# Kernel tuning notes

Hardware: AMD Instinct MI355X
Metric: run time of the kernel (lower is better)

## Reference

```python
import jax, jax.numpy as jnp
import numpy as np

EPS = 1e-8
LOSS_EPS = 1e-6
LOSS_WEIGHT = 1.0
N_BOXES = 262144

# ---------- rotated-2D-box helpers (mmcv diff_iou_rotated style) ----------

def box2corners_2d(box):
    # box: (N,5) = (x, y, w, h, alpha) -> corners (N,4,2), CCW order
    x, y, w, h, a = box[:, 0], box[:, 1], box[:, 2], box[:, 3], box[:, 4]
    x4 = jnp.array([0.5, -0.5, -0.5, 0.5], box.dtype) * w[:, None]   # (N,4)
    y4 = jnp.array([0.5, 0.5, -0.5, -0.5], box.dtype) * h[:, None]
    c, s = jnp.cos(a)[:, None], jnp.sin(a)[:, None]
    rx = x4 * c - y4 * s + x[:, None]
    ry = x4 * s + y4 * c + y[:, None]
    return jnp.stack([rx, ry], axis=-1)


def box_intersection(c1, c2):
    # segment-segment intersections between the 4 edges of each box
    # c1, c2: (N,4,2) -> pts (N,16,2), mask (N,16)
    l1 = jnp.concatenate([c1, jnp.roll(c1, -1, axis=1)], axis=-1)[:, :, None, :]  # (N,4,1,4)
    l2 = jnp.concatenate([c2, jnp.roll(c2, -1, axis=1)], axis=-1)[:, None, :, :]  # (N,1,4,4)
    x1, y1, x2, y2 = l1[..., 0], l1[..., 1], l1[..., 2], l1[..., 3]
    x3, y3, x4, y4 = l2[..., 0], l2[..., 1], l2[..., 2], l2[..., 3]
    num = (y4 - y3) * (x2 - x1) - (x4 - x3) * (y2 - y1)
    den_t = (x4 - x3) * (y1 - y3) - (y4 - y3) * (x1 - x3)
    den_u = (x2 - x1) * (y1 - y3) - (y2 - y1) * (x1 - x3)
    safe = jnp.where(num == 0.0, 1.0, num)
    t = jnp.where(num == 0.0, -1.0, den_t / safe)
    u = jnp.where(num == 0.0, -1.0, -den_u / safe)
    mask = (t > 0.0) & (t < 1.0) & (u > 0.0) & (u < 1.0)  # (N,4,4)
    t2 = den_t / (num + EPS)
    pts = jnp.stack([x1 + t2 * (x2 - x1), y1 + t2 * (y2 - y1)], axis=-1)
    pts = pts * mask[..., None]
    n = c1.shape[0]
    return pts.reshape(n, 16, 2), mask.reshape(n, 16)


def box_in_box(c1, c2):
    # which corners of box1 lie inside box2; c1,c2: (N,4,2) -> (N,4) bool
    a, b, d = c2[:, 0:1], c2[:, 1:2], c2[:, 3:4]
    ab, ad, am = b - a, d - a, c1 - a
    p_ab = jnp.sum(ab * am, -1) / jnp.sum(ab * ab, -1)
    p_ad = jnp.sum(ad * am, -1) / jnp.sum(ad * ad, -1)
    tol = 1e-6
    return (p_ab > -tol) & (p_ab < 1 + tol) & (p_ad > -tol) & (p_ad < 1 + tol)


def polygon_area(vertices, mask):
    # sort valid vertices CCW around their mean, close polygon, shoelace area
    # vertices: (N,24,2), mask: (N,24) bool -> area (N,)
    maskf = mask.astype(vertices.dtype)
    nv = jnp.maximum(jnp.sum(maskf, axis=1, keepdims=True), 1.0)
    mean = jnp.sum(vertices * maskf[..., None], axis=1, keepdims=True) / nv[..., None]
    v = vertices - mean
    ang = jnp.arctan2(v[..., 1], v[..., 0])
    # invalid vertices get huge, index-increasing keys so they sort last (stable)
    ang = jnp.where(mask, ang, 1e6 + jnp.arange(24, dtype=vertices.dtype))
    order = jnp.argsort(ang, axis=1)                         # (N,24) int
    vs = jnp.take_along_axis(v, order[..., None], axis=1)    # (N,24,2)
    ms = jnp.take_along_axis(mask, order, axis=1)
    first = vs[:, 0:1]                                       # first (valid) vertex
    vs = jnp.where(ms[..., None], vs, first)                 # pad closes polygon
    x, y = vs[..., 0], vs[..., 1]
    xn, yn = jnp.roll(x, -1, axis=1), jnp.roll(y, -1, axis=1)
    return 0.5 * jnp.abs(jnp.sum(x * yn - y * xn, axis=1))


def diff_iou_rotated_3d(b1, b2):
    # b1, b2: (N,7) = (x,y,z,w,h,l,alpha) -> IoU3D (N,)
    c1 = box2corners_2d(b1[:, jnp.array([0, 1, 3, 4, 6])])
    c2 = box2corners_2d(b2[:, jnp.array([0, 1, 3, 4, 6])])
    ipts, imask = box_intersection(c1, c2)
    m12 = box_in_box(c1, c2)
    m21 = box_in_box(c2, c1)
    vertices = jnp.concatenate([c1, c2, ipts], axis=1)   # (N,24,2)
    mask = jnp.concatenate([m12, m21, imask], axis=1)    # (N,24)
    inter_2d = polygon_area(vertices, mask)
    zmax1, zmin1 = b1[:, 2] + 0.5 * b1[:, 5], b1[:, 2] - 0.5 * b1[:, 5]
    zmax2, zmin2 = b2[:, 2] + 0.5 * b2[:, 5], b2[:, 2] - 0.5 * b2[:, 5]
    z_ov = jnp.maximum(jnp.minimum(zmax1, zmax2) - jnp.maximum(zmin1, zmin2), 0.0)
    inter_3d = inter_2d * z_ov
    vol1 = b1[:, 3] * b1[:, 4] * b1[:, 5]
    vol2 = b2[:, 3] * b2[:, 4] * b2[:, 5]
    return inter_3d / (vol1 + vol2 - inter_3d)


def corners_from_bboxes3d(b):
    # (N,7) -> (N,8,3); rotation about axis=1 (mmdet3d rotation_3d_in_axis)
    corners_norm = jnp.array([[-0.5, -0.5, -0.5], [-0.5, -0.5, 0.5],
                              [-0.5, 0.5, 0.5], [-0.5, 0.5, -0.5],
                              [0.5, -0.5, -0.5], [0.5, -0.5, 0.5],
                              [0.5, 0.5, 0.5], [0.5, 0.5, -0.5]], b.dtype)
    corners = corners_norm[None] * b[:, None, 3:6]          # (N,8,3)
    c, s = jnp.cos(b[:, 6])[:, None], jnp.sin(b[:, 6])[:, None]
    x, y, z = corners[..., 0], corners[..., 1], corners[..., 2]
    xr = x * c + z * s
    zr = -x * s + z * c
    return jnp.stack([xr, y, zr], axis=-1) + b[:, None, :3]


def diou_3d_loss(pred, target):
    iou3d = jnp.nan_to_num(diff_iou_rotated_3d(pred, target), nan=0.0)
    ctd = jnp.sum((pred[:, :3] - target[:, :3]) ** 2, axis=-1)
    cnd = jnp.mean(jnp.sum((corners_from_bboxes3d(pred)
                            - corners_from_bboxes3d(target)) ** 2, axis=-1), axis=1)
    did = jnp.sum(target[:, 3:6] ** 2, axis=-1)
    return 1.0 - iou3d + (ctd + cnd) / (ctd + cnd + did + LOSS_EPS)


def setup_inputs() -> dict:
    key = jax.random.key(0)
    k1, k2, k3, k4, k5 = jax.random.split(key, 5)
    xy = jax.random.uniform(k1, (N_BOXES, 2), minval=-40.0, maxval=40.0)
    z = jax.random.uniform(k2, (N_BOXES, 1), minval=-3.0, maxval=1.0)
    dims = jax.random.uniform(k3, (N_BOXES, 3), minval=0.8, maxval=4.0)
    ang = jax.random.uniform(k4, (N_BOXES, 1), minval=-np.pi, maxval=np.pi)
    target = jnp.concatenate([xy, z, dims, ang], axis=1).astype(jnp.float32)
    noise = jax.random.normal(k5, (N_BOXES, 7), jnp.float32) * \
        jnp.array([0.3, 0.3, 0.1, 0.2, 0.2, 0.2, 0.1], jnp.float32)
    pred = target + noise
    pred = pred.at[:, 3:6].set(jnp.maximum(pred[:, 3:6], 0.1))
    return {"pred": pred, "target": target}


def reference(pred, target):
    # DIOU3DLoss.forward with weight=None, reduction='mean'
    return LOSS_WEIGHT * jnp.mean(diou_3d_loss(pred, target))
```

## Files before the change

### kernel.cpp

```cpp
#include <hip/hip_runtime.h>
#include <math.h>

#define EPSI 1e-8f
#define TOLI 1e-6f

__device__ __forceinline__ float frcp(float x) { return __builtin_amdgcn_rcpf(x); }

#define CE(A, B) {                                  \
    unsigned ka = key[A], kb = key[B];              \
    key[A] = ka < kb ? ka : kb;                     \
    key[B] = ka < kb ? kb : ka; }

__global__ __launch_bounds__(256) void diou3d_main(
    const float* __restrict__ pred, const float* __restrict__ tgt,
    float* __restrict__ partial, int n)
{
    __shared__ float2 vbuf[24][256];
    __shared__ float wsum[4];
    int tx = threadIdx.x;
    int tid = blockIdx.x * 256 + tx;
    float loss = 0.0f;
    if (tid < n) {
        const float* P = pred + (size_t)tid * 7;
        const float* T = tgt  + (size_t)tid * 7;
        float p0 = P[0], p1 = P[1], p2 = P[2], p3 = P[3], p4 = P[4], p5 = P[5], p6 = P[6];
        float t0 = T[0], t1 = T[1], t2 = T[2], t3 = T[3], t4 = T[4], t5 = T[5], t6 = T[6];

        float sp, cp, st, ct;
        __sincosf(p6, &sp, &cp);
        __sincosf(t6, &st, &ct);
        const float hx[4] = {0.5f, -0.5f, -0.5f, 0.5f};
        const float hy[4] = {0.5f, 0.5f, -0.5f, -0.5f};
        float c1x[4], c1y[4], c2x[4], c2y[4];
#pragma unroll
        for (int k = 0; k < 4; k++) {
            float xa = hx[k] * p3, ya = hy[k] * p4;
            c1x[k] = xa * cp - ya * sp + p0;
            c1y[k] = xa * sp + ya * cp + p1;
            float xb = hx[k] * t3, yb = hy[k] * t4;
            c2x[k] = xb * ct - yb * st + t0;
            c2y[k] = xb * st + yb * ct + t1;
        }

        float vx[24], vy[24];
        bool  vm[24];

        {
            float abx = c2x[1] - c2x[0], aby = c2y[1] - c2y[0];
            float adx = c2x[3] - c2x[0], ady = c2y[3] - c2y[0];
            float rab = frcp(abx * abx + aby * aby);
            float rad = frcp(adx * adx + ady * ady);
#pragma unroll
            for (int k = 0; k < 4; k++) {
                float amx = c1x[k] - c2x[0], amy = c1y[k] - c2y[0];
                float pab = (abx * amx + aby * amy) * rab;
                float pad = (adx * amx + ady * amy) * rad;
                vm[k] = (pab > -TOLI) && (pab < 1.0f + TOLI) && (pad > -TOLI) && (pad < 1.0f + TOLI);
                vx[k] = c1x[k]; vy[k] = c1y[k];
            }
        }
        {
            float abx = c1x[1] - c1x[0], aby = c1y[1] - c1y[0];
            float adx = c1x[3] - c1x[0], ady = c1y[3] - c1y[0];
            float rab = frcp(abx * abx + aby * aby);
            float rad = frcp(adx * adx + ady * ady);
#pragma unroll
            for (int k = 0; k < 4; k++) {
                float amx = c2x[k] - c1x[0], amy = c2y[k] - c1y[0];
                float pab = (abx * amx + aby * amy) * rab;
                float pad = (adx * amx + ady * amy) * rad;
                vm[4 + k] = (pab > -TOLI) && (pab < 1.0f + TOLI) && (pad > -TOLI) && (pad < 1.0f + TOLI);
                vx[4 + k] = c2x[k]; vy[4 + k] = c2y[k];
            }
        }

#pragma unroll
        for (int i = 0; i < 4; i++) {
            float x1 = c1x[i], y1 = c1y[i];
            float dx12 = c1x[(i + 1) & 3] - x1, dy12 = c1y[(i + 1) & 3] - y1;
#pragma unroll
            for (int j = 0; j < 4; j++) {
                float x3 = c2x[j], y3 = c2y[j];
                float dx34 = c2x[(j + 1) & 3] - x3, dy34 = c2y[(j + 1) & 3] - y3;
                float num  = dy34 * dx12 - dx34 * dy12;
                float dxs = x1 - x3, dys = y1 - y3;
                float den_t = dx34 * dys - dy34 * dxs;
                float den_u = dx12 * dys - dy12 * dxs;
                bool m = (den_t * num > 0.0f) && ((num - den_t) * num > 0.0f)
                      && (den_u * num < 0.0f) && ((num + den_u) * num > 0.0f);
                float t2d = den_t * frcp(num + EPSI);
                int idx = 8 + i * 4 + j;
                vx[idx] = x1 + t2d * dx12;
                vy[idx] = y1 + t2d * dy12;
                vm[idx] = m;
            }
        }

        float cntf = 0.0f, sx = 0.0f, sy = 0.0f;
#pragma unroll
        for (int k = 0; k < 24; k++) {
            cntf += vm[k] ? 1.0f : 0.0f;
            sx   += vm[k] ? vx[k] : 0.0f;
            sy   += vm[k] ? vy[k] : 0.0f;
        }
        int ic = (int)cntf;
        float rnv = frcp(fmaxf(cntf, 1.0f));
        float mx = sx * rnv, my = sy * rnv;

        unsigned key[24];
#pragma unroll
        for (int k = 0; k < 24; k++) {
            float ux = vx[k] - mx, uy = vy[k] - my;
            vbuf[k][tx] = make_float2(ux, uy);
            float d = fabsf(ux) + fabsf(uy);
            float pq = ux * frcp(d);
            pq = (d == 0.0f) ? 0.0f : pq;
            float ang = (uy < 0.0f) ? (pq - 1.0f) : (1.0f - pq);
            unsigned u = __float_as_uint(ang);
            u ^= (unsigned)(((int)u >> 31)) | 0x80000000u;
            unsigned kk = (u & 0xFFFFFFE0u) | (unsigned)k;
            key[k] = vm[k] ? kk : (0xFFFFFFE0u | (unsigned)k);
        }

#pragma unroll
        for (int p = 1; p < 32; p <<= 1) {
#pragma unroll
            for (int k = p; k >= 1; k >>= 1) {
#pragma unroll
                for (int j = k & (p - 1); j + k < 32; j += 2 * k) {
#pragma unroll
                    for (int i = 0; i < k; i++) {
                        int lo = i + j, hi = i + j + k;
                        if (hi < 24 && (lo / (2 * p) == hi / (2 * p))) {
                            CE(lo, hi);
                        }
                    }
                }
            }
        }

        float gx[12], gy[12];
#pragma unroll
        for (int s = 0; s < 12; s++) {
            int idx = (int)(key[s] & 31u);
            float2 v = vbuf[idx][tx];
            gx[s] = v.x; gy[s] = v.y;
        }

        float x0 = gx[0], y0 = gy[0];
#pragma unroll
        for (int s = 0; s < 12; s++) {
            bool v = (s < ic);
            gx[s] = v ? gx[s] : x0;
            gy[s] = v ? gy[s] : y0;
        }
        float area2 = 0.0f;
#pragma unroll
        for (int s = 0; s < 12; s++) {
            int ns = (s == 11) ? 0 : s + 1;
            area2 += gx[s] * gy[ns] - gy[s] * gx[ns];
        }
        float inter2d = 0.5f * fabsf(area2);

        float zmax1 = p2 + 0.5f * p5, zmin1 = p2 - 0.5f * p5;
        float zmax2 = t2 + 0.5f * t5, zmin2 = t2 - 0.5f * t5;
        float zov = fmaxf(fminf(zmax1, zmax2) - fmaxf(zmin1, zmin2), 0.0f);
        float inter3d = inter2d * zov;
        float vol1 = p3 * p4 * p5, vol2 = t3 * t4 * t5;
        float iou = inter3d / (vol1 + vol2 - inter3d);
        if (isnan(iou)) iou = 0.0f;

        float d0 = p0 - t0, d1 = p1 - t1, d2 = p2 - t2;
        float ctd = d0 * d0 + d1 * d1 + d2 * d2;

        float cosd = cp * ct + sp * st;
        float dp2 = p3 * p3 + p4 * p4 + p5 * p5;
        float dt2 = t3 * t3 + t4 * t4 + t5 * t5;
        float crossd = p3 * t3 * cosd + p4 * t4 + p5 * t5 * cosd;
        float cnd = ctd + 0.25f * (dp2 + dt2) - 0.5f * crossd;

        float dterm = (ctd + cnd) / (ctd + cnd + dt2 + 1e-6f);
        loss = 1.0f - iou + dterm;
    }

#pragma unroll
    for (int off = 32; off > 0; off >>= 1) loss += __shfl_down(loss, off);
    int lane = tx & 63, wid = tx >> 6;
    if (lane == 0) wsum[wid] = loss;
    __syncthreads();
    if (tx == 0)
        partial[blockIdx.x] = wsum[0] + wsum[1] + wsum[2] + wsum[3];
}

__global__ __launch_bounds__(256) void diou3d_reduce(
    const float* __restrict__ partial, int nblocks, float* __restrict__ out, float invn)
{
    float s = 0.0f;
    for (int i = threadIdx.x; i < nblocks; i += 256) s += partial[i];
#pragma unroll
    for (int off = 32; off > 0; off >>= 1) s += __shfl_down(s, off);
    __shared__ float wsum[4];
    int lane = threadIdx.x & 63, wid = threadIdx.x >> 6;
    if (lane == 0) wsum[wid] = s;
    __syncthreads();
    if (threadIdx.x == 0)
        out[0] = (wsum[0] + wsum[1] + wsum[2] + wsum[3]) * invn;
}

extern "C" void kernel_launch(void* const* d_in, const int* in_sizes, int n_in,
                              void* d_out, int out_size, void* d_ws, size_t ws_size,
                              hipStream_t stream) {
    const float* pred = (const float*)d_in[0];
    const float* tgt  = (const float*)d_in[1];
    float* out = (float*)d_out;
    int n = in_sizes[0] / 7;
    const int T = 256;
    int blocks = (n + T - 1) / T;
    float* partial = (float*)d_ws;
    diou3d_main<<<blocks, T, 0, stream>>>(pred, tgt, partial, n);
    diou3d_reduce<<<1, 256, 0, stream>>>(partial, blocks, out, 1.0f / (float)n);
}
```

Baseline: 76.04 us.

## Pack centered vertices as fp16 pairs in LDS and raise occupancy bound

Stores the mean-centered polygon vertices in shared memory as packed fp16 pairs instead of float2, halving LDS footprint per block (48KB to 24KB) so more blocks fit per CU. It also adds a min-blocks hint of 5 to launch_bounds and replaces boolean masks with float multipliers used in FMAs. The fp16 rounding of vertex coordinates reduces area precision, so the shoelace sum carries larger error than the fp32 reference.

```diff
diff --git a/kernel.cpp b/kernel.cpp
--- a/kernel.cpp
+++ b/kernel.cpp
@@ -3,6 +3,8 @@
 
 #define EPSI 1e-8f
 #define TOLI 1e-6f
+
+typedef __fp16 half2v __attribute__((ext_vector_type(2)));
 
 __device__ __forceinline__ float frcp(float x) { return __builtin_amdgcn_rcpf(x); }
 
@@ -11,11 +13,11 @@
     key[A] = ka < kb ? ka : kb;                     \
     key[B] = ka < kb ? kb : ka; }
 
-__global__ __launch_bounds__(256) void diou3d_main(
+__global__ __launch_bounds__(256, 5) void diou3d_main(
     const float* __restrict__ pred, const float* __restrict__ tgt,
     float* __restrict__ partial, int n)
 {
-    __shared__ float2 vbuf[24][256];
+    __shared__ unsigned vbuf[24][256];
     __shared__ float wsum[4];
     int tx = threadIdx.x;
     int tid = blockIdx.x * 256 + tx;
@@ -43,7 +45,7 @@
         }
 
         float vx[24], vy[24];
-        bool  vm[24];
+        float ma[24];
 
         {
             float abx = c2x[1] - c2x[0], aby = c2y[1] - c2y[0];
@@ -55,7 +57,8 @@
                 float amx = c1x[k] - c2x[0], amy = c1y[k] - c2y[0];
                 float pab = (abx * amx + aby * amy) * rab;
                 float pad = (adx * amx + ady * amy) * rad;
-                vm[k] = (pab > -TOLI) && (pab < 1.0f + TOLI) && (pad > -TOLI) && (pad < 1.0f + TOLI);
+                bool m = (pab > -TOLI) && (pab < 1.0f + TOLI) && (pad > -TOLI) && (pad < 1.0f + TOLI);
+                ma[k] = m ? 1.0f : 0.0f;
                 vx[k] = c1x[k]; vy[k] = c1y[k];
             }
         }
@@ -69,7 +72,8 @@
                 float amx = c2x[k] - c1x[0], amy = c2y[k] - c1y[0];
                 float pab = (abx * amx + aby * amy) * rab;
                 float pad = (adx * amx + ady * amy) * rad;
-                vm[4 + k] = (pab > -TOLI) && (pab < 1.0f + TOLI) && (pad > -TOLI) && (pad < 1.0f + TOLI);
+                bool m = (pab > -TOLI) && (pab < 1.0f + TOLI) && (pad > -TOLI) && (pad < 1.0f + TOLI);
+                ma[4 + k] = m ? 1.0f : 0.0f;
                 vx[4 + k] = c2x[k]; vy[4 + k] = c2y[k];
             }
         }
@@ -92,16 +96,16 @@
                 int idx = 8 + i * 4 + j;
                 vx[idx] = x1 + t2d * dx12;
                 vy[idx] = y1 + t2d * dy12;
-                vm[idx] = m;
+                ma[idx] = m ? 1.0f : 0.0f;
             }
         }
 
         float cntf = 0.0f, sx = 0.0f, sy = 0.0f;
 #pragma unroll
         for (int k = 0; k < 24; k++) {
-            cntf += vm[k] ? 1.0f : 0.0f;
-            sx   += vm[k] ? vx[k] : 0.0f;
-            sy   += vm[k] ? vy[k] : 0.0f;
+            cntf += ma[k];
+            sx = fmaf(ma[k], vx[k], sx);
+            sy = fmaf(ma[k], vy[k], sy);
         }
         int ic = (int)cntf;
         float rnv = frcp(fmaxf(cntf, 1.0f));
@@ -111,7 +115,8 @@
 #pragma unroll
         for (int k = 0; k < 24; k++) {
             float ux = vx[k] - mx, uy = vy[k] - my;
-            vbuf[k][tx] = make_float2(ux, uy);
+            half2v h = __builtin_amdgcn_cvt_pkrtz(ux, uy);
+            vbuf[k][tx] = __builtin_bit_cast(unsigned, h);
             float d = fabsf(ux) + fabsf(uy);
             float pq = ux * frcp(d);
             pq = (d == 0.0f) ? 0.0f : pq;
@@ -119,7 +124,7 @@
             unsigned u = __float_as_uint(ang);
             u ^= (unsigned)(((int)u >> 31)) | 0x80000000u;
             unsigned kk = (u & 0xFFFFFFE0u) | (unsigned)k;
-            key[k] = vm[k] ? kk : (0xFFFFFFE0u | (unsigned)k);
+            key[k] = (ma[k] != 0.0f) ? kk : (0xFFFFFFE0u | (unsigned)k);
         }
 
 #pragma unroll
@@ -143,8 +148,8 @@
 #pragma unroll
         for (int s = 0; s < 12; s++) {
             int idx = (int)(key[s] & 31u);
-            float2 v = vbuf[idx][tx];
-            gx[s] = v.x; gy[s] = v.y;
+            half2v h = __builtin_bit_cast(half2v, vbuf[idx][tx]);
+            gx[s] = (float)h.x; gy[s] = (float)h.y;
         }
 
         float x0 = gx[0], y0 = gy[0];
```

Measured after the change: 101.6 us. 1.34x slower.
